# Optimization experiments

Hardware: AMD Instinct MI355X
Metric: run time of the kernel (lower is better)

## Reference

```python
import jax, jax.numpy as jnp
import numpy as np

N = 131072      # total nodes (128 graphs * 1024 nodes)
E = 1048576     # edges (avg degree 8)
IN = 256        # in_channels
H = 128         # hidden_channels (hardcoded 128 pad in source)
OUT = 64        # out_channels (dec_hid_dim)
G = 128         # num graphs == hidden_channels -> no padding branch
NPG = N // G    # nodes per graph


def setup_inputs() -> dict:
    key = jax.random.key(0)
    ks = jax.random.split(key, 32)
    def p(k, shape, fan):
        return (jax.random.normal(k, shape, jnp.float32) / np.sqrt(fan)).astype(jnp.float32)
    inp = {}
    inp["x"] = jax.random.normal(ks[0], (N, IN), jnp.float32)
    inp["edge_index"] = jax.random.randint(ks[1], (2, E), 0, N, dtype=jnp.int32)
    inp["batch"] = (jnp.arange(N, dtype=jnp.int32) // NPG).astype(jnp.int32)
    # GATConv layers: W, att_src, att_dst, bias
    inp["W1"], inp["as1"], inp["ad1"], inp["b1"] = p(ks[2], (IN, H), IN), p(ks[3], (H,), H), p(ks[4], (H,), H), jnp.zeros((H,), jnp.float32)
    inp["W2"], inp["as2"], inp["ad2"], inp["b2"] = p(ks[5], (H, H), H), p(ks[6], (H,), H), p(ks[7], (H,), H), jnp.zeros((H,), jnp.float32)
    inp["W3"], inp["as3"], inp["ad3"], inp["b3"] = p(ks[8], (H, H), H), p(ks[9], (H,), H), p(ks[10], (H,), H), jnp.zeros((H,), jnp.float32)
    # lin_news, lin0, lin1
    inp["Wn"], inp["bn"] = p(ks[11], (IN, H), IN), jnp.zeros((H,), jnp.float32)
    inp["W0"], inp["b0"] = p(ks[12], (H, H), H), jnp.zeros((H,), jnp.float32)
    inp["Wl"], inp["bl"] = p(ks[13], (2 * H, OUT), 2 * H), jnp.zeros((OUT,), jnp.float32)
    # attention_1 / attention_2: attn Linear(2H -> OUT) + v Linear(OUT -> 1, no bias)
    inp["Wa1"], inp["ba1"], inp["v1"] = p(ks[14], (2 * H, OUT), 2 * H), jnp.zeros((OUT,), jnp.float32), p(ks[15], (OUT,), OUT)
    inp["Wa2"], inp["ba2"], inp["v2"] = p(ks[16], (2 * H, OUT), 2 * H), jnp.zeros((OUT,), jnp.float32), p(ks[17], (OUT,), OUT)
    return inp


def _gat_layer(x, src, dst, W, a_src, a_dst, b):
    # single-head PyG GATConv (self-loops already appended to src/dst)
    h = x @ W                                   # [N, H]
    es = h @ a_src                              # [N]
    ed = h @ a_dst                              # [N]
    e = jax.nn.leaky_relu(es[src] + ed[dst], 0.2)   # [E+N]
    m = jax.ops.segment_max(e, dst, num_segments=N)
    ex = jnp.exp(e - m[dst])
    den = jax.ops.segment_sum(ex, dst, num_segments=N)
    alpha = ex / (den[dst] + 1e-16)
    out = jax.ops.segment_sum(alpha[:, None] * h[src], dst, num_segments=N)
    return out + b


def _bahdanau(hidden, enc, Wa, ba, v):
    # energy[i,j] = tanh([hidden_i; enc_j] @ Wa + ba) @ v   -> [B, B]
    Hdim = hidden.shape[1]
    eh = hidden @ Wa[:Hdim]        # [B, OUT]
    ee = enc @ Wa[Hdim:]           # [B, OUT]
    energy = jnp.tanh(eh[:, None, :] + ee[None, :, :] + ba)  # [B, B, OUT]
    return energy @ v              # [B, B]


def reference(x, edge_index, batch,
              W1, as1, ad1, b1, W2, as2, ad2, b2, W3, as3, ad3, b3,
              Wn, bn, W0, b0, Wl, bl, Wa1, ba1, v1, Wa2, ba2, v2):
    loops = jnp.arange(N, dtype=edge_index.dtype)
    src = jnp.concatenate([edge_index[0], loops])
    dst = jnp.concatenate([edge_index[1], loops])
    h = jax.nn.relu(_gat_layer(x, src, dst, W1, as1, ad1, b1))
    h = jax.nn.relu(_gat_layer(h, src, dst, W2, as2, ad2, b2))
    h = jax.nn.relu(_gat_layer(h, src, dst, W3, as3, ad3, b3))
    h = jax.ops.segment_max(h, batch, num_segments=G)        # global max pool [G, H]
    h = jax.nn.relu(h @ W0 + b0)
    # root node = first node index of each (sorted) graph
    root = jax.ops.segment_min(jnp.arange(N, dtype=jnp.int32), batch, num_segments=G)
    news = jax.nn.relu(x[root] @ Wn + bn)                    # [G, H]
    fused_h = _bahdanau(h, news, Wa1, ba1, v1)               # [G, G]
    fused_news = _bahdanau(news, h, Wa2, ba2, v2)            # [G, G]
    out = jnp.concatenate([fused_h, fused_news], axis=-1)    # [G, 2G] == [128, 256]
    out = out.reshape(-1, 2 * H) @ Wl + bl                   # [G, OUT]
    return jax.nn.sigmoid(out)
```

## Files before the change

### kernel.cpp

```cpp
#include <hip/hip_runtime.h>

#define N_NODES 131072
#define N_EDGES 1048576
#define TOT_EDG (N_NODES + N_EDGES)
#define G_GRAPHS 128
#define NPG 1024

typedef unsigned short u16;
typedef unsigned int u32;
typedef __attribute__((ext_vector_type(8))) short bh8;
typedef __attribute__((ext_vector_type(4))) float f4;

__device__ __forceinline__ float bcf(u32 u){ return __builtin_bit_cast(float, u); }
__device__ __forceinline__ u32 bcu(float f){ return __builtin_bit_cast(u32, f); }

__device__ __forceinline__ u16 f2b(float f){ return (u16)((bcu(f) + 0x8000u) >> 16); }
__device__ __forceinline__ u32 pk_rn(float lo, float hi){
    u32 a = bcu(lo) + 0x8000u;
    u32 b = bcu(hi) + 0x8000u;
    return __builtin_amdgcn_perm(b, a, 0x07060302u);
}

__global__ void wtrans_all(const float* __restrict__ W1, const float* __restrict__ W2,
                           const float* __restrict__ W3,
                           u16* __restrict__ Wt1, u16* __restrict__ Wt2, u16* __restrict__ Wt3){
    int b = blockIdx.x, t = threadIdx.x;
    if (b < 128){
        int idx = b*256 + t; int c = idx >> 8, k = idx & 255;
        Wt1[idx] = f2b(W1[k*128 + c]);
    } else if (b < 192){
        int idx = (b-128)*256 + t; int c = idx >> 7, k = idx & 127;
        Wt2[idx] = f2b(W2[k*128 + c]);
    } else {
        int idx = (b-192)*256 + t; int c = idx >> 7, k = idx & 127;
        Wt3[idx] = f2b(W3[k*128 + c]);
    }
}

__global__ void k_init(int* cnt){ cnt[blockIdx.x*256 + threadIdx.x] = 1; }

__global__ void k_count(const int* __restrict__ dst, int* cnt){
    int e = blockIdx.x*256 + threadIdx.x;
    atomicAdd(&cnt[dst[e]], 1);
}

__global__ void k_blocksum(const int* __restrict__ cnt, int* bsum){
    int b = blockIdx.x, t = threadIdx.x;
    int base = b*1024 + t*4;
    int s = cnt[base] + cnt[base+1] + cnt[base+2] + cnt[base+3];
    __shared__ int red[256];
    red[t] = s; __syncthreads();
    for (int off = 128; off > 0; off >>= 1){
        if (t < off) red[t] += red[t+off];
        __syncthreads();
    }
    if (t == 0) bsum[b] = red[0];
}

__global__ void k_scanblock(int* bsum){
    int t = threadIdx.x;
    __shared__ int l[128];
    int v = bsum[t];
    l[t] = v; __syncthreads();
    for (int off = 1; off < 128; off <<= 1){
        int u = (t >= off) ? l[t-off] : 0;
        __syncthreads();
        l[t] += u;
        __syncthreads();
    }
    bsum[t] = l[t] - v;
}

__global__ void k_scan(const int* __restrict__ cnt, const int* __restrict__ bsum,
                       int* row_ptr, int* col, int* cur){
    int b = blockIdx.x, t = threadIdx.x;
    int base = b*1024 + t*4;
    int c0 = cnt[base], c1 = cnt[base+1], c2 = cnt[base+2], c3 = cnt[base+3];
    int s = c0+c1+c2+c3;
    __shared__ int l[256];
    l[t] = s; __syncthreads();
    for (int off = 1; off < 256; off <<= 1){
        int v = (t >= off) ? l[t-off] : 0;
        __syncthreads();
        l[t] += v;
        __syncthreads();
    }
    int e0 = l[t] - s + bsum[b];
    int e1 = e0 + c0, e2 = e1 + c1, e3 = e2 + c2;
    row_ptr[base] = e0;   col[e0] = base;   cur[base]   = e0 + 1;
    row_ptr[base+1] = e1; col[e1] = base+1; cur[base+1] = e1 + 1;
    row_ptr[base+2] = e2; col[e2] = base+2; cur[base+2] = e2 + 1;
    row_ptr[base+3] = e3; col[e3] = base+3; cur[base+3] = e3 + 1;
    if (b == 127 && t == 255) row_ptr[N_NODES] = TOT_EDG;
}

__global__ void k_scatter(const int* __restrict__ src, const int* __restrict__ dst,
                          int* cur, int* col){
    int e = blockIdx.x*256 + threadIdx.x;
    int p = atomicAdd(&cur[dst[e]], 1);
    col[p] = src[e];
}

template<int K, bool AF32>
__global__ __launch_bounds__(256) void gat_gemm(const void* __restrict__ A_,
                                                const u16* __restrict__ Bt,
                                                const float* __restrict__ asrc,
                                                const float* __restrict__ adst,
                                                u16* __restrict__ Hb,
                                                float* __restrict__ es, float* __restrict__ ed){
    constexpr int SA = 40;
    __shared__ u16 As[128*SA];
    __shared__ u16 Bs[128*SA];
    const int t = threadIdx.x;
    const int wave = t >> 6, lane = t & 63, quad = lane >> 4, m16 = lane & 15;
    const long rowBase = (long)blockIdx.x * 128;
    const int r = t >> 1, c0 = (t & 1) * 16;
    f4 acc[2][8] = {};

    for (int kk = 0; kk < K; kk += 32){
        if (AF32){
            const float* A = (const float*)A_;
            const float* src = A + (rowBase + r) * (long)K + kk + c0;
            float4 a0 = *(const float4*)(src+0);
            float4 a1 = *(const float4*)(src+4);
            float4 a2 = *(const float4*)(src+8);
            float4 a3 = *(const float4*)(src+12);
            uint4 v0, v1;
            v0.x = pk_rn(a0.x, a0.y); v0.y = pk_rn(a0.z, a0.w);
            v0.z = pk_rn(a1.x, a1.y); v0.w = pk_rn(a1.z, a1.w);
            v1.x = pk_rn(a2.x, a2.y); v1.y = pk_rn(a2.z, a2.w);
            v1.z = pk_rn(a3.x, a3.y); v1.w = pk_rn(a3.z, a3.w);
            *(uint4*)&As[r*SA + c0]     = v0;
            *(uint4*)&As[r*SA + c0 + 8] = v1;
        } else {
            const u16* A = (const u16*)A_;
            const u16* src = A + (rowBase + r) * (long)K + kk + c0;
            uint4 v0 = *(const uint4*)(src);
            uint4 v1 = *(const uint4*)(src + 8);
            *(uint4*)&As[r*SA + c0]     = v0;
            *(uint4*)&As[r*SA + c0 + 8] = v1;
        }
        {
            const u16* src = Bt + r * (long)K + kk + c0;
            uint4 v0 = *(const uint4*)(src);
            uint4 v1 = *(const uint4*)(src + 8);
            *(uint4*)&Bs[r*SA + c0]     = v0;
            *(uint4*)&Bs[r*SA + c0 + 8] = v1;
        }
        __syncthreads();
        bh8 af0 = *(const bh8*)&As[(wave*32      + m16)*SA + quad*8];
        bh8 af1 = *(const bh8*)&As[(wave*32 + 16 + m16)*SA + quad*8];
        #pragma unroll
        for (int ct = 0; ct < 8; ct++){
            bh8 bw = *(const bh8*)&Bs[(ct*16 + m16)*SA + quad*8];
            acc[0][ct] = __builtin_amdgcn_mfma_f32_16x16x32_bf16(bw, af0, acc[0][ct], 0,0,0);
            acc[1][ct] = __builtin_amdgcn_mfma_f32_16x16x32_bf16(bw, af1, acc[1][ct], 0,0,0);
        }
        __syncthreads();
    }
    #pragma unroll
    for (int nt2 = 0; nt2 < 2; nt2++){
        long node = rowBase + wave*32 + nt2*16 + m16;
        float ps = 0.f, pd = 0.f;
        #pragma unroll
        for (int ct = 0; ct < 8; ct++){
            f4 a = acc[nt2][ct];
            float4 av = *(const float4*)(asrc + ct*16 + quad*4);
            float4 dv = *(const float4*)(adst + ct*16 + quad*4);
            ps += a.x*av.x + a.y*av.y + a.z*av.z + a.w*av.w;
            pd += a.x*dv.x + a.y*dv.y + a.z*dv.z + a.w*dv.w;
            uint2 o;
            o.x = pk_rn(a.x, a.y);
            o.y = pk_rn(a.z, a.w);
            *(uint2*)(Hb + node*128 + ct*16 + quad*4) = o;
        }
        ps += __shfl_xor(ps, 16); ps += __shfl_xor(ps, 32);
        pd += __shfl_xor(pd, 16); pd += __shfl_xor(pd, 32);
        if (quad == 0){ es[node] = ps; ed[node] = pd; }
    }
}

__global__ __launch_bounds__(256) void gat_agg(const u16* __restrict__ Hb,
                        const float* __restrict__ es, const float* __restrict__ ed,
                        const int* __restrict__ row_ptr, const int* __restrict__ colv,
                        const float* __restrict__ bias, u16* __restrict__ Xb){
    int t = threadIdx.x, wave = t >> 6, lane = t & 63;
    int grp = lane >> 4, cl = lane & 15;
    int n = blockIdx.x * 4 + wave;
    int beg = row_ptr[n], end = row_ptr[n+1];
    float edn = ed[n];
    float den = 0.f;
    float a[8] = {};
    for (int j = beg + grp; j < end; j += 4){
        int s = colv[j];
        float e = es[s] + edn;
        e = fmaxf(e, 0.f) + 0.2f*fminf(e, 0.f);
        float ex = __expf(e);
        uint4 hv = *(const uint4*)(Hb + (long)s*128 + cl*8);
        den += ex;
        a[0] += ex * bcf(hv.x << 16);  a[1] += ex * bcf(hv.x & 0xffff0000u);
        a[2] += ex * bcf(hv.y << 16);  a[3] += ex * bcf(hv.y & 0xffff0000u);
        a[4] += ex * bcf(hv.z << 16);  a[5] += ex * bcf(hv.z & 0xffff0000u);
        a[6] += ex * bcf(hv.w << 16);  a[7] += ex * bcf(hv.w & 0xffff0000u);
    }
    #pragma unroll
    for (int k = 0; k < 8; k++){
        a[k] += __shfl_xor(a[k], 16);
        a[k] += __shfl_xor(a[k], 32);
    }
    den += __shfl_xor(den, 16); den += __shfl_xor(den, 32);
    if (grp == 0){
        float inv = 1.0f / (den + 1e-16f);
        float4 b0 = *(const float4*)(bias + cl*8);
        float4 b1 = *(const float4*)(bias + cl*8 + 4);
        uint4 ov;
        ov.x = pk_rn(fmaxf(a[0]*inv + b0.x, 0.f), fmaxf(a[1]*inv + b0.y, 0.f));
        ov.y = pk_rn(fmaxf(a[2]*inv + b0.z, 0.f), fmaxf(a[3]*inv + b0.w, 0.f));
        ov.z = pk_rn(fmaxf(a[4]*inv + b1.x, 0.f), fmaxf(a[5]*inv + b1.y, 0.f));
        ov.w = pk_rn(fmaxf(a[6]*inv + b1.z, 0.f), fmaxf(a[7]*inv + b1.w, 0.f));
        *(uint4*)(Xb + (long)n*128 + cl*8) = ov;
    }
}

__global__ void pool_part(const u16* __restrict__ Xb, float* __restrict__ pooled8){
    int b = blockIdx.x;
    int t = threadIdx.x;
    int wave = t >> 6, lane = t & 63, grp = lane >> 4, cl = lane & 15;
    long base = (long)b * 128;
    float m[8] = {};
    for (int i = 0; i < 8; i++){
        long node = base + wave*32 + i*4 + grp;
        uint4 hv = *(const uint4*)(Xb + node*128 + cl*8);
        m[0] = fmaxf(m[0], bcf(hv.x << 16));  m[1] = fmaxf(m[1], bcf(hv.x & 0xffff0000u));
        m[2] = fmaxf(m[2], bcf(hv.y << 16));  m[3] = fmaxf(m[3], bcf(hv.y & 0xffff0000u));
        m[4] = fmaxf(m[4], bcf(hv.z << 16));  m[5] = fmaxf(m[5], bcf(hv.z & 0xffff0000u));
        m[6] = fmaxf(m[6], bcf(hv.w << 16));  m[7] = fmaxf(m[7], bcf(hv.w & 0xffff0000u));
    }
    #pragma unroll
    for (int k = 0; k < 8; k++){
        m[k] = fmaxf(m[k], __shfl_xor(m[k], 16));
        m[k] = fmaxf(m[k], __shfl_xor(m[k], 32));
    }
    __shared__ float red[4][128];
    if (grp == 0){
        #pragma unroll
        for (int k = 0; k < 8; k++) red[wave][cl*8 + k] = m[k];
    }
    __syncthreads();
    if (t < 128){
        float v = fmaxf(fmaxf(red[0][t], red[1][t]), fmaxf(red[2][t], red[3][t]));
        pooled8[(long)b*128 + t] = v;
    }
}

__global__ void tail2(const float* __restrict__ x, const float* __restrict__ pooled8,
                      const float* __restrict__ Wn, const float* __restrict__ bn,
                      const float* __restrict__ W0, const float* __restrict__ b0,
                      const float* __restrict__ Wa1, const float* __restrict__ Wa2,
                      float* eh1, float* ee1, float* eh2, float* ee2){
    int g = blockIdx.x, c = threadIdx.x;
    __shared__ float xr[256], pr[128], nr[128], hr[128];
    const float* xroot = x + (size_t)g * NPG * 256;
    xr[c] = xroot[c]; xr[c+128] = xroot[c+128];
    {
        const float* pg = pooled8 + (long)g*8*128 + c;
        float v = pg[0];
        for (int s2 = 1; s2 < 8; s2++) v = fmaxf(v, pg[s2*128]);
        pr[c] = v;
    }
    __syncthreads();
    float a = bn[c];
    for (int k = 0; k < 256; k++) a += xr[k] * Wn[k*128 + c];
    a = fmaxf(a, 0.f);
    float b = b0[c];
    for (int k = 0; k < 128; k++) b += pr[k] * W0[k*128 + c];
    b = fmaxf(b, 0.f);
    nr[c] = a; hr[c] = b;
    __syncthreads();
    if (c < 64){
        int o = c; float s1 = 0.f, s2 = 0.f;
        for (int k = 0; k < 128; k++){ s1 += hr[k]*Wa1[k*64 + o]; s2 += nr[k]*Wa2[k*64 + o]; }
        eh1[g*64 + o] = s1; eh2[g*64 + o] = s2;
    } else {
        int o = c - 64; float s1 = 0.f, s2 = 0.f;
        for (int k = 0; k < 128; k++){ s1 += nr[k]*Wa1[(128+k)*64 + o]; s2 += hr[k]*Wa2[(128+k)*64 + o]; }
        ee1[g*64 + o] = s1; ee2[g*64 + o] = s2;
    }
}

__global__ void tail3(const float* __restrict__ eh1, const float* __restrict__ ee1,
                      const float* __restrict__ eh2, const float* __restrict__ ee2,
                      const float* __restrict__ ba1, const float* __restrict__ v1,
                      const float* __restrict__ ba2, const float* __restrict__ v2,
                      const float* __restrict__ Wl, const float* __restrict__ bl,
                      float* out){
    int i = blockIdx.x, t = threadIdx.x;
    __shared__ float e1i[64], e2i[64], fh[128], fn[128];
    if (t < 64) e1i[t] = eh1[i*64 + t];
    else if (t < 128) e2i[t-64] = eh2[i*64 + (t-64)];
    __syncthreads();
    if (t < 128){
        int j = t; float s = 0.f;
        for (int o = 0; o < 64; o++) s += tanhf(e1i[o] + ee1[j*64+o] + ba1[o]) * v1[o];
        fh[j] = s;
    } else {
        int j = t - 128; float s = 0.f;
        for (int o = 0; o < 64; o++) s += tanhf(e2i[o] + ee2[j*64+o] + ba2[o]) * v2[o];
        fn[j] = s;
    }
    __syncthreads();
    if (t < 64){
        int o = t; float s = bl[o];
        for (int j = 0; j < 128; j++) s += fh[j]*Wl[j*64+o] + fn[j]*Wl[(128+j)*64+o];
        out[i*64 + o] = 1.0f / (1.0f + expf(-s));
    }
}

extern "C" void kernel_launch(void* const* d_in, const int* in_sizes, int n_in,
                              void* d_out, int out_size, void* d_ws, size_t ws_size,
                              hipStream_t stream){
    const float* x   = (const float*)d_in[0];
    const int* eidx  = (const int*)d_in[1];
    const int* esrc  = eidx;
    const int* edst  = eidx + N_EDGES;
    const float* W1  = (const float*)d_in[3];
    const float* as1 = (const float*)d_in[4];
    const float* ad1 = (const float*)d_in[5];
    const float* b1  = (const float*)d_in[6];
    const float* W2  = (const float*)d_in[7];
    const float* as2 = (const float*)d_in[8];
    const float* ad2 = (const float*)d_in[9];
    const float* b2  = (const float*)d_in[10];
    const float* W3  = (const float*)d_in[11];
    const float* as3 = (const float*)d_in[12];
    const float* ad3 = (const float*)d_in[13];
    const float* b3  = (const float*)d_in[14];
    const float* Wn  = (const float*)d_in[15];
    const float* bn  = (const float*)d_in[16];
    const float* W0  = (const float*)d_in[17];
    const float* b0  = (const float*)d_in[18];
    const float* Wl  = (const float*)d_in[19];
    const float* bl  = (const float*)d_in[20];
    const float* Wa1 = (const float*)d_in[21];
    const float* ba1 = (const float*)d_in[22];
    const float* v1  = (const float*)d_in[23];
    const float* Wa2 = (const float*)d_in[24];
    const float* ba2 = (const float*)d_in[25];
    const float* v2  = (const float*)d_in[26];
    float* out = (float*)d_out;

    char* p = (char*)d_ws;
    auto take = [&](size_t b)->char*{ char* q = p; p += (b + 255) & ~(size_t)255; return q; };
    u16* Hb      = (u16*)take((size_t)N_NODES*128*2);
    u16* Xb      = (u16*)take((size_t)N_NODES*128*2);
    float* es    = (float*)take((size_t)N_NODES*4);
    float* ed    = (float*)take((size_t)N_NODES*4);
    int* cnt     = (int*)take((size_t)N_NODES*4);
    int* row_ptr = (int*)take((size_t)(N_NODES+1)*4);
    int* colb    = (int*)take((size_t)TOT_EDG*4);
    int* bsum    = (int*)take(128*4);
    u16* Wt1     = (u16*)take(128*256*2);
    u16* Wt2     = (u16*)take(128*128*2);
    u16* Wt3     = (u16*)take(128*128*2);
    float* pooled8=(float*)take((size_t)1024*128*4);
    float* eh1   = (float*)take(128*64*4);
    float* ee1   = (float*)take(128*64*4);
    float* eh2   = (float*)take(128*64*4);
    float* ee2   = (float*)take(128*64*4);

    wtrans_all<<<256, 256, 0, stream>>>(W1, W2, W3, Wt1, Wt2, Wt3);

    k_init<<<N_NODES/256, 256, 0, stream>>>(cnt);
    k_count<<<N_EDGES/256, 256, 0, stream>>>(edst, cnt);
    k_blocksum<<<128, 256, 0, stream>>>(cnt, bsum);
    k_scanblock<<<1, 128, 0, stream>>>(bsum);
    k_scan<<<128, 256, 0, stream>>>(cnt, bsum, row_ptr, colb, cnt );
    k_scatter<<<N_EDGES/256, 256, 0, stream>>>(esrc, edst, cnt, colb);

    gat_gemm<256, true><<<N_NODES/128, 256, 0, stream>>>(x, Wt1, as1, ad1, Hb, es, ed);
    gat_agg<<<N_NODES/4, 256, 0, stream>>>(Hb, es, ed, row_ptr, colb, b1, Xb);
    gat_gemm<128, false><<<N_NODES/128, 256, 0, stream>>>(Xb, Wt2, as2, ad2, Hb, es, ed);
    gat_agg<<<N_NODES/4, 256, 0, stream>>>(Hb, es, ed, row_ptr, colb, b2, Xb);
    gat_gemm<128, false><<<N_NODES/128, 256, 0, stream>>>(Xb, Wt3, as3, ad3, Hb, es, ed);
    gat_agg<<<N_NODES/4, 256, 0, stream>>>(Hb, es, ed, row_ptr, colb, b3, Xb);

    pool_part<<<1024, 256, 0, stream>>>(Xb, pooled8);
    tail2<<<G_GRAPHS, 128, 0, stream>>>(x, pooled8, Wn, bn, W0, b0, Wa1, Wa2, eh1, ee1, eh2, ee2);
    tail3<<<G_GRAPHS, 256, 0, stream>>>(eh1, ee1, eh2, ee2, ba1, v1, ba2, v2, Wl, bl, out);
}
```

Before: 670.6 us.

## Build CSR via two-level bucket sort with shared-memory atomics; unroll aggregation loop

Replaces the global-atomic count and scatter CSR construction with a two-pass binning scheme. Edges are first bucketed by destination graph (1024-node buckets) using LDS histograms and a scan, then each bucket builds its local CSR with shared-memory atomics. The aim is to cut contended random global atomics and scattered writes. The aggregation loop is also unrolled by two so two neighbour row loads are in flight at once. The cost is an extra edge buffer and more kernel launches, and bucket_csr runs on only 128 blocks, which may leave the GPU underused.

```diff
diff --git a/kernel.cpp b/kernel.cpp
--- a/kernel.cpp
+++ b/kernel.cpp
@@ -37,30 +37,44 @@
     }
 }
 
-__global__ void k_init(int* cnt){ cnt[blockIdx.x*256 + threadIdx.x] = 1; }
-
-__global__ void k_count(const int* __restrict__ dst, int* cnt){
-    int e = blockIdx.x*256 + threadIdx.x;
-    atomicAdd(&cnt[dst[e]], 1);
-}
-
-__global__ void k_blocksum(const int* __restrict__ cnt, int* bsum){
+
+__global__ __launch_bounds__(256) void bin_hist(const int* __restrict__ dst, int* __restrict__ hist){
+    __shared__ int h[128];
     int b = blockIdx.x, t = threadIdx.x;
-    int base = b*1024 + t*4;
-    int s = cnt[base] + cnt[base+1] + cnt[base+2] + cnt[base+3];
-    __shared__ int red[256];
-    red[t] = s; __syncthreads();
-    for (int off = 128; off > 0; off >>= 1){
-        if (t < off) red[t] += red[t+off];
-        __syncthreads();
-    }
-    if (t == 0) bsum[b] = red[0];
-}
-
-__global__ void k_scanblock(int* bsum){
+    if (t < 128) h[t] = 0;
+    __syncthreads();
+    int base = b*1024 + t;
+    #pragma unroll
+    for (int i = 0; i < 4; i++) atomicAdd(&h[dst[base + i*256] >> 10], 1);
+    __syncthreads();
+    if (t < 128) hist[b*128 + t] = h[t];
+}
+
+__global__ __launch_bounds__(256) void bin_scan(const int* __restrict__ hist,
+                                                int* __restrict__ baseRel, int* __restrict__ total){
+    int bk = blockIdx.x, t = threadIdx.x;
+    int v[4]; int s = 0;
+    #pragma unroll
+    for (int i = 0; i < 4; i++){ v[i] = hist[(t*4+i)*128 + bk]; s += v[i]; }
+    __shared__ int l[256];
+    l[t] = s; __syncthreads();
+    for (int off = 1; off < 256; off <<= 1){
+        int u = (t >= off) ? l[t-off] : 0;
+        __syncthreads();
+        l[t] += u;
+        __syncthreads();
+    }
+    int run = l[t] - s;
+    #pragma unroll
+    for (int i = 0; i < 4; i++){ baseRel[(t*4+i)*128 + bk] = run; run += v[i]; }
+    if (t == 255) total[bk] = run;
+}
+
+__global__ void bucket_scan(const int* __restrict__ total, int* __restrict__ bstart,
+                            int* __restrict__ brow, int* __restrict__ row_ptr){
     int t = threadIdx.x;
     __shared__ int l[128];
-    int v = bsum[t];
+    int v = total[t];
     l[t] = v; __syncthreads();
     for (int off = 1; off < 128; off <<= 1){
         int u = (t >= off) ? l[t-off] : 0;
@@ -68,37 +82,71 @@
         l[t] += u;
         __syncthreads();
     }
-    bsum[t] = l[t] - v;
-}
-
-__global__ void k_scan(const int* __restrict__ cnt, const int* __restrict__ bsum,
-                       int* row_ptr, int* col, int* cur){
+    int e = l[t] - v;
+    bstart[t] = e;
+    brow[t] = e + t*1024;
+    if (t == 127) row_ptr[N_NODES] = TOT_EDG;
+}
+
+__global__ __launch_bounds__(256) void bin_scatter(const int* __restrict__ src, const int* __restrict__ dst,
+                           const int* __restrict__ baseRel, const int* __restrict__ bstart,
+                           uint2* __restrict__ binned){
+    __shared__ int cur[128];
+    __shared__ int bs[128];
     int b = blockIdx.x, t = threadIdx.x;
-    int base = b*1024 + t*4;
-    int c0 = cnt[base], c1 = cnt[base+1], c2 = cnt[base+2], c3 = cnt[base+3];
-    int s = c0+c1+c2+c3;
+    if (t < 128){ cur[t] = baseRel[b*128 + t]; bs[t] = bstart[t]; }
+    __syncthreads();
+    #pragma unroll
+    for (int i = 0; i < 4; i++){
+        int e = b*1024 + i*256 + t;
+        int s = src[e], d = dst[e];
+        int bk = d >> 10;
+        int r = atomicAdd(&cur[bk], 1);
+        uint2 o; o.x = (u32)s; o.y = (u32)d;
+        binned[bs[bk] + r] = o;
+    }
+}
+
+__global__ __launch_bounds__(256) void bucket_csr(const uint2* __restrict__ binned,
+                           const int* __restrict__ bstart, const int* __restrict__ total,
+                           const int* __restrict__ brow,
+                           int* __restrict__ row_ptr, int* __restrict__ colb){
+    int b = blockIdx.x, t = threadIdx.x;
+    __shared__ int cnt[1024];
     __shared__ int l[256];
+    int ebeg = bstart[b], ecnt = total[b], rbase = brow[b];
+    for (int i = t; i < 1024; i += 256) cnt[i] = 1;
+    __syncthreads();
+    for (int i = t; i < ecnt; i += 256){
+        uint2 e = binned[ebeg + i];
+        atomicAdd(&cnt[e.y & 1023], 1);
+    }
+    __syncthreads();
+    int v0 = cnt[t*4], v1 = cnt[t*4+1], v2 = cnt[t*4+2], v3 = cnt[t*4+3];
+    int s = v0+v1+v2+v3;
     l[t] = s; __syncthreads();
     for (int off = 1; off < 256; off <<= 1){
-        int v = (t >= off) ? l[t-off] : 0;
-        __syncthreads();
-        l[t] += v;
-        __syncthreads();
-    }
-    int e0 = l[t] - s + bsum[b];
-    int e1 = e0 + c0, e2 = e1 + c1, e3 = e2 + c2;
-    row_ptr[base] = e0;   col[e0] = base;   cur[base]   = e0 + 1;
-    row_ptr[base+1] = e1; col[e1] = base+1; cur[base+1] = e1 + 1;
-    row_ptr[base+2] = e2; col[e2] = base+2; cur[base+2] = e2 + 1;
-    row_ptr[base+3] = e3; col[e3] = base+3; cur[base+3] = e3 + 1;
-    if (b == 127 && t == 255) row_ptr[N_NODES] = TOT_EDG;
-}
-
-__global__ void k_scatter(const int* __restrict__ src, const int* __restrict__ dst,
-                          int* cur, int* col){
-    int e = blockIdx.x*256 + threadIdx.x;
-    int p = atomicAdd(&cur[dst[e]], 1);
-    col[p] = src[e];
+        int u = (t >= off) ? l[t-off] : 0;
+        __syncthreads();
+        l[t] += u;
+        __syncthreads();
+    }
+    int excl = l[t] - s;
+    int node0 = b*1024 + t*4;
+    int p0 = rbase + excl;
+    int p1 = p0 + v0, p2 = p1 + v1, p3 = p2 + v2;
+    row_ptr[node0]   = p0; colb[p0] = node0;
+    row_ptr[node0+1] = p1; colb[p1] = node0+1;
+    row_ptr[node0+2] = p2; colb[p2] = node0+2;
+    row_ptr[node0+3] = p3; colb[p3] = node0+3;
+    __syncthreads();
+    cnt[t*4] = p0+1; cnt[t*4+1] = p1+1; cnt[t*4+2] = p2+1; cnt[t*4+3] = p3+1;
+    __syncthreads();
+    for (int i = t; i < ecnt; i += 256){
+        uint2 e = binned[ebeg + i];
+        int p = atomicAdd(&cnt[e.y & 1023], 1);
+        colb[p] = (int)e.x;
+    }
 }
 
 template<int K, bool AF32>
@@ -191,7 +239,26 @@
     float edn = ed[n];
     float den = 0.f;
     float a[8] = {};
-    for (int j = beg + grp; j < end; j += 4){
+    int j = beg + grp;
+    for (; j + 4 < end; j += 8){
+        int s0 = colv[j], s1 = colv[j+4];
+        float q0 = es[s0] + edn, q1 = es[s1] + edn;
+        uint4 h0 = *(const uint4*)(Hb + (long)s0*128 + cl*8);
+        uint4 h1 = *(const uint4*)(Hb + (long)s1*128 + cl*8);
+        q0 = fmaxf(q0, 0.f) + 0.2f*fminf(q0, 0.f);
+        q1 = fmaxf(q1, 0.f) + 0.2f*fminf(q1, 0.f);
+        float x0 = __expf(q0), x1 = __expf(q1);
+        den += x0 + x1;
+        a[0] += x0*bcf(h0.x << 16) + x1*bcf(h1.x << 16);
+        a[1] += x0*bcf(h0.x & 0xffff0000u) + x1*bcf(h1.x & 0xffff0000u);
+        a[2] += x0*bcf(h0.y << 16) + x1*bcf(h1.y << 16);
+        a[3] += x0*bcf(h0.y & 0xffff0000u) + x1*bcf(h1.y & 0xffff0000u);
+        a[4] += x0*bcf(h0.z << 16) + x1*bcf(h1.z << 16);
+        a[5] += x0*bcf(h0.z & 0xffff0000u) + x1*bcf(h1.z & 0xffff0000u);
+        a[6] += x0*bcf(h0.w << 16) + x1*bcf(h1.w << 16);
+        a[7] += x0*bcf(h0.w & 0xffff0000u) + x1*bcf(h1.w & 0xffff0000u);
+    }
+    if (j < end){
         int s = colv[j];
         float e = es[s] + edn;
         e = fmaxf(e, 0.f) + 0.2f*fminf(e, 0.f);
@@ -355,10 +422,14 @@
     u16* Xb      = (u16*)take((size_t)N_NODES*128*2);
     float* es    = (float*)take((size_t)N_NODES*4);
     float* ed    = (float*)take((size_t)N_NODES*4);
-    int* cnt     = (int*)take((size_t)N_NODES*4);
     int* row_ptr = (int*)take((size_t)(N_NODES+1)*4);
     int* colb    = (int*)take((size_t)TOT_EDG*4);
-    int* bsum    = (int*)take(128*4);
+    uint2* binned= (uint2*)take((size_t)N_EDGES*8);
+    int* hist    = (int*)take((size_t)1024*128*4);
+    int* baseRel = (int*)take((size_t)1024*128*4);
+    int* total   = (int*)take(128*4);
+    int* bstart  = (int*)take(128*4);
+    int* brow    = (int*)take(128*4);
     u16* Wt1     = (u16*)take(128*256*2);
     u16* Wt2     = (u16*)take(128*128*2);
     u16* Wt3     = (u16*)take(128*128*2);
@@ -370,12 +441,11 @@
 
     wtrans_all<<<256, 256, 0, stream>>>(W1, W2, W3, Wt1, Wt2, Wt3);
 
-    k_init<<<N_NODES/256, 256, 0, stream>>>(cnt);
-    k_count<<<N_EDGES/256, 256, 0, stream>>>(edst, cnt);
-    k_blocksum<<<128, 256, 0, stream>>>(cnt, bsum);
-    k_scanblock<<<1, 128, 0, stream>>>(bsum);
-    k_scan<<<128, 256, 0, stream>>>(cnt, bsum, row_ptr, colb, cnt );
-    k_scatter<<<N_EDGES/256, 256, 0, stream>>>(esrc, edst, cnt, colb);
+    bin_hist<<<1024, 256, 0, stream>>>(edst, hist);
+    bin_scan<<<128, 256, 0, stream>>>(hist, baseRel, total);
+    bucket_scan<<<1, 128, 0, stream>>>(total, bstart, brow, row_ptr);
+    bin_scatter<<<1024, 256, 0, stream>>>(esrc, edst, baseRel, bstart, binned);
+    bucket_csr<<<128, 256, 0, stream>>>(binned, bstart, total, brow, row_ptr, colb);
 
     gat_gemm<256, true><<<N_NODES/128, 256, 0, stream>>>(x, Wt1, as1, ad1, Hb, es, ed);
     gat_agg<<<N_NODES/4, 256, 0, stream>>>(Hb, es, ed, row_ptr, colb, b1, Xb);
```

Result: faster. 577.0 us (-14.0%).
